# Optimization experiments

Hardware: AMD Instinct MI355X
Metric: run time of the kernel (lower is better)

The kernel has to match this reference:

```python
import jax, jax.numpy as jnp
import numpy as np

N = 100000      # num_nodes
E = 1600000     # num edges (avg degree 16)
R = 400         # num_relations passed to GCNLayer (masks at R and 2R)
DIN, DH, DOUT = 128, 128, 128
EPS = 1e-5


def setup_inputs() -> dict:
    key = jax.random.key(0)
    ks = jax.random.split(key, 8)
    src = jax.random.randint(ks[0], (E,), 0, N)
    dst = jax.random.randint(ks[1], (E,), 0, N)
    rel = jax.random.randint(ks[2], (E,), 0, 2 * R + 1)  # covers orig/inverse/self-loop buckets
    edges = jnp.stack([src, rel, dst], axis=1)  # [E,3] = (head, rel, tail)

    def xinit(k, shape, fan_in):
        return jax.random.normal(k, shape, jnp.float32) * (1.0 / np.sqrt(fan_in))

    node_emb = xinit(ks[3], (N, DIN), DIN)
    # stacked relation-branch linears: [3, out, in] = (original, inverse, self_loop)
    W1 = xinit(ks[4], (3, DH, DIN), DIN)
    b1 = jnp.zeros((3, DH), jnp.float32)
    Ws1 = xinit(ks[5], (DH, DIN), DIN)
    bs1 = jnp.zeros((DH,), jnp.float32)
    g1 = jnp.ones((DH,), jnp.float32)
    be1 = jnp.zeros((DH,), jnp.float32)
    W2 = xinit(ks[6], (3, DOUT, DH), DH)
    b2 = jnp.zeros((3, DOUT), jnp.float32)
    Ws2 = xinit(ks[7], (DOUT, DH), DH)
    bs2 = jnp.zeros((DOUT,), jnp.float32)
    g2 = jnp.ones((DOUT,), jnp.float32)
    be2 = jnp.zeros((DOUT,), jnp.float32)
    return dict(edges=edges, node_emb=node_emb, W1=W1, b1=b1, Ws1=Ws1, bs1=bs1,
                g1=g1, be1=be1, W2=W2, b2=b2, Ws2=Ws2, bs2=bs2, g2=g2, be2=be2)


def _gcn_layer(x, src, dst, bucket, W, b):
    # Project node features once per relation branch (same math as projecting
    # gathered src features, but N << E so this is cheaper): Y[r] = x @ W[r].T + b[r]
    Y = jnp.einsum('nd,rod->rno', x, W) + b[:, None, :]     # [3, N, out]
    msgs = Y[bucket, src]                                   # [E, out] gather by (branch, src)
    n = x.shape[0]
    out = jax.ops.segment_sum(msgs, dst, num_segments=n)    # scatter-add to dst
    cnt = jax.ops.segment_sum(jnp.ones_like(dst, dtype=x.dtype), dst, num_segments=n)
    out = out / jnp.maximum(cnt, 1.0)[:, None]              # degree norm, clamp min=1
    return jax.nn.relu(out)


def _layer_norm(x, g, b):
    m = jnp.mean(x, axis=-1, keepdims=True)
    v = jnp.mean((x - m) ** 2, axis=-1, keepdims=True)
    return (x - m) * jax.lax.rsqrt(v + EPS) * g + b


def reference(edges, node_emb, W1, b1, Ws1, bs1, g1, be1, W2, b2, Ws2, bs2, g2, be2):
    src, rel, dst = edges[:, 0], edges[:, 1], edges[:, 2]
    # bucket: 0=original (rel<R), 1=inverse (R<=rel<2R), 2=self-loop (rel>=2R)
    bucket = (rel >= R).astype(jnp.int32) + (rel >= 2 * R).astype(jnp.int32)

    x1 = _gcn_layer(node_emb, src, dst, bucket, W1, b1)
    x1 = x1 + node_emb @ Ws1.T + bs1                # skip1
    x1 = _layer_norm(x1, g1, be1)                   # dropout: eval-mode identity

    x2 = _gcn_layer(x1, src, dst, bucket, W2, b2)
    x2 = x2 + x1 @ Ws2.T + bs2                      # skip2
    x2 = _layer_norm(x2, g2, be2)
    return x2
```

## Files before the change

### kernel.cpp

```cpp
#include <hip/hip_runtime.h>
#include <stdint.h>

typedef unsigned int uint;
typedef unsigned short ushort;

#define NNODES 100000
#define NPAD   100096
#define NEDGES 1600000
#define RCONST 400
#define CAP    64
#define ZROW   NNODES

#define NBKT   196
#define NBLK_A 512
#define EPB    3125
#define RUNCAP 64

typedef __attribute__((ext_vector_type(8))) short short8;
typedef __attribute__((ext_vector_type(4))) float f32x4;

__device__ __forceinline__ float bflo(uint u){ union{uint i;float f;}c; c.i=u<<16; return c.f; }
__device__ __forceinline__ float bfhi(uint u){ union{uint i;float f;}c; c.i=u&0xFFFF0000u; return c.f; }
__device__ __forceinline__ ushort f2bf(float f){ union{uint i;float ff;}c; c.ff=f; uint u=c.i;
    return (ushort)((u + 0x7FFFu + ((u>>16)&1u))>>16); }
__device__ __forceinline__ uint pack2(float lo, float hi){
    return (uint)f2bf(lo) | ((uint)f2bf(hi)<<16); }


__global__ __launch_bounds__(256) void binfill_kernel(const int* __restrict__ edges,
                                                      int* __restrict__ runcnt,
                                                      uint* __restrict__ binned) {
    __shared__ int pos[NBKT];
    int blk = blockIdx.x, tid = threadIdx.x;
    for (int i = tid; i < NBKT; i += 256) pos[i] = 0;
    __syncthreads();
    int start = blk * EPB;
    for (int i = tid; i < EPB; i += 256) {
        int e = start + i;
        int src = edges[e * 3];
        int rel = edges[e * 3 + 1];
        int dst = edges[e * 3 + 2];
        int bkt = (rel >= RCONST) + (rel >= 2 * RCONST);
        int b = dst >> 9, off = dst & 511;
        int p = atomicAdd(&pos[b], 1);
        if (p < RUNCAP)
            binned[((size_t)b * NBLK_A + blk) * RUNCAP + p] =
                (uint)src | ((uint)bkt << 17) | ((uint)off << 19);
    }
    __syncthreads();
    for (int i = tid; i < NBKT; i += 256)
        runcnt[blk * NBKT + i] = min(pos[i], RUNCAP);
}


__global__ __launch_bounds__(256) void scatter_kernel(const uint* __restrict__ binned,
                                                      const int* __restrict__ runcnt,
                                                      int* __restrict__ elist,
                                                      uint* __restrict__ segp,
                                                      float4* __restrict__ cnts) {
    __shared__ int cnt3[512][4];
    __shared__ int cur[512][4];
    int b = blockIdx.x, tid = threadIdx.x;
    int base = b << 9;
    for (int i = tid; i < 512; i += 256) { cnt3[i][0] = 0; cnt3[i][1] = 0; cnt3[i][2] = 0; }
    __syncthreads();
    #pragma unroll
    for (int rr = 0; rr < 2; ++rr) {
        int r = tid * 2 + rr;
        int n = runcnt[r * NBKT + b];
        const uint* p = binned + ((size_t)b * NBLK_A + r) * RUNCAP;
        for (int i = 0; i < n; ++i) {
            uint e = p[i];
            atomicAdd(&cnt3[e >> 19][(e >> 17) & 3], 1);
        }
    }
    __syncthreads();
    for (int i = tid; i < 512; i += 256) {
        int node = base + i;
        if (node >= NPAD) continue;
        int c0 = cnt3[i][0], c1 = cnt3[i][1], c2 = cnt3[i][2];
        int n0 = min((c0 + 1) & ~1, 64);
        int n1 = min((c1 + 1) & ~1, 64 - n0);
        int n2 = min((c2 + 1) & ~1, 64 - n0 - n1);
        int s1 = n0, s2 = n0 + n1;
        cur[i][0] = 0; cur[i][1] = s1; cur[i][2] = s2;
        int* er = elist + (size_t)node * 64;
        for (int j = min(c0, n0); j < n0; ++j) er[j] = ZROW;
        for (int j = min(c1, n1); j < n1; ++j) er[s1 + j] = ZROW;
        for (int j = min(c2, n2); j < n2; ++j) er[s2 + j] = ZROW;
        cnt3[i][0] = s1; cnt3[i][1] = s2; cnt3[i][2] = s2 + n2;
        segp[node] = (uint)n0 | ((uint)n1 << 8) | ((uint)n2 << 16);
        float4 v;
        v.x = (float)c0; v.y = (float)c1; v.z = (float)c2;
        v.w = 1.0f / fmaxf((float)(c0 + c1 + c2), 1.0f);
        cnts[node] = v;
    }
    __syncthreads();
    #pragma unroll
    for (int rr = 0; rr < 2; ++rr) {
        int r = tid * 2 + rr;
        int n = runcnt[r * NBKT + b];
        const uint* p = binned + ((size_t)b * NBLK_A + r) * RUNCAP;
        for (int i = 0; i < n; ++i) {
            uint e = p[i];
            int off = (int)(e >> 19), bk = (int)((e >> 17) & 3);
            int pos = atomicAdd(&cur[off][bk], 1);
            if (pos < cnt3[off][bk])
                elist[(size_t)(base + off) * 64 + pos] = (int)(e & 0x7FFFFu);
        }
    }
}


__global__ __launch_bounds__(256) void convx_kernel(const float* __restrict__ x,
                                                    uint* __restrict__ xb) {
    size_t i = (size_t)blockIdx.x * 256 + threadIdx.x;
    if (i < (size_t)NPAD * 64) {
        uint val = 0;
        if (i < (size_t)NNODES * 64) {
            float2 f = *(const float2*)&x[i * 2];
            val = pack2(f.x, f.y);
        }
        xb[i] = val;
    }
}

__global__ __launch_bounds__(256) void wconv_kernel(const float* __restrict__ W,
                                                    const float* __restrict__ Ws,
                                                    uint* __restrict__ Wb) {
    int i = blockIdx.x * 256 + threadIdx.x;
    if (i < 128 * 256) {
        int n = i >> 8, kp = i & 255, k = kp * 2;
        float v0, v1;
        if (k < 384) {
            int r = k >> 7, kk = k & 127;
            const float* p = W + r * 16384 + n * 128 + kk;
            v0 = p[0]; v1 = p[1];
        } else {
            const float* p = Ws + n * 128 + (k - 384);
            v0 = p[0]; v1 = p[1];
        }
        Wb[i] = pack2(v0, v1);
    }
}


template<bool OUT_BF16>
__global__ __launch_bounds__(512, 2) void fused_kernel(
    const uint* __restrict__ xbu,
    const ushort* __restrict__ Wb,
    const uint* __restrict__ segp,
    const int*  __restrict__ elist,
    const float4* __restrict__ cnts,
    const float* __restrict__ bia,
    const float* __restrict__ bs,
    const float* __restrict__ g,
    const float* __restrict__ be,
    void* __restrict__ out) {
    __shared__ ushort lA[64 * 384];
    __shared__ ushort lB[128 * 64];
    __shared__ float sS1[4][64], sS2[4][64];
    __shared__ float sMean[64], sRstd[64];

    const ushort* xbs = (const ushort*)xbu;
    int tid = threadIdx.x;
    int w = tid >> 6, lane = tid & 63;
    int wm = w >> 2, wn = w & 3;
    int quad = lane >> 4, l15 = lane & 15;
    int node0 = blockIdx.x * 64;
    uint swzR = (uint)((l15 & 7) << 4);

    int brow = tid >> 2, bseg2 = (tid & 3) * 2;
    uint swzB = (uint)((brow & 7) << 4);
    uint4 rb0, rb1;
    auto loadB = [&](int t) {
        const ushort* pb = Wb + t * 64 + (size_t)brow * 512 + bseg2 * 8;
        rb0 = *(const uint4*)(pb);
        rb1 = *(const uint4*)(pb + 8);
    };
    auto storeB = [&]() {
        char* bB = (char*)lB + brow * 128;
        *(uint4*)(bB + (((uint)(bseg2 * 16)) ^ swzB))       = rb0;
        *(uint4*)(bB + (((uint)((bseg2 + 1) * 16)) ^ swzB)) = rb1;
    };

    loadB(0);

    for (int i = 0; i < 8; ++i) {
        int arow = w * 8 + i;
        int node = node0 + arow;
        uint sp = segp[node];
        int tot = (int)(sp & 255) + (int)((sp >> 8) & 255) + (int)((sp >> 16) & 255);
        float inv = cnts[node].w;
        int ve = elist[(size_t)node * 64 + lane];

        float a0l = 0.f, a0h = 0.f, a1l = 0.f, a1h = 0.f, a2l = 0.f, a2h = 0.f;
        int j = 0;
        for (; j + 4 <= tot; j += 4) {
            int e0 = __builtin_amdgcn_readlane(ve, j);
            int e1 = __builtin_amdgcn_readlane(ve, j + 1);
            int e2 = __builtin_amdgcn_readlane(ve, j + 2);
            int e3 = __builtin_amdgcn_readlane(ve, j + 3);
            int s0 = e0 & 0x1FFFF, k0 = e0 >> 17;
            int s1 = e1 & 0x1FFFF, k1 = e1 >> 17;
            int s2 = e2 & 0x1FFFF, k2 = e2 >> 17;
            int s3 = e3 & 0x1FFFF, k3 = e3 >> 17;
            uint u0 = xbu[((size_t)s0 << 6) + lane];
            uint u1 = xbu[((size_t)s1 << 6) + lane];
            uint u2 = xbu[((size_t)s2 << 6) + lane];
            uint u3 = xbu[((size_t)s3 << 6) + lane];

            float q00 = (k0 == 0) ? 1.f : 0.f, q01 = (k0 == 1) ? 1.f : 0.f, q02 = (k0 == 2) ? 1.f : 0.f;
            float q10 = (k1 == 0) ? 1.f : 0.f, q11 = (k1 == 1) ? 1.f : 0.f, q12 = (k1 == 2) ? 1.f : 0.f;
            float q20 = (k2 == 0) ? 1.f : 0.f, q21 = (k2 == 1) ? 1.f : 0.f, q22 = (k2 == 2) ? 1.f : 0.f;
            float q30 = (k3 == 0) ? 1.f : 0.f, q31 = (k3 == 1) ? 1.f : 0.f, q32 = (k3 == 2) ? 1.f : 0.f;

            float f0l = bflo(u0), f0h = bfhi(u0);
            float f1l = bflo(u1), f1h = bfhi(u1);
            float f2l = bflo(u2), f2h = bfhi(u2);
            float f3l = bflo(u3), f3h = bfhi(u3);

            a0l = fmaf(q00, f0l, a0l); a1l = fmaf(q01, f0l, a1l); a2l = fmaf(q02, f0l, a2l);
            a0h = fmaf(q00, f0h, a0h); a1h = fmaf(q01, f0h, a1h); a2h = fmaf(q02, f0h, a2h);
            a0l = fmaf(q10, f1l, a0l); a1l = fmaf(q11, f1l, a1l); a2l = fmaf(q12, f1l, a2l);
            a0h = fmaf(q10, f1h, a0h); a1h = fmaf(q11, f1h, a1h); a2h = fmaf(q12, f1h, a2h);
            a0l = fmaf(q20, f2l, a0l); a1l = fmaf(q21, f2l, a1l); a2l = fmaf(q22, f2l, a2l);
            a0h = fmaf(q20, f2h, a0h); a1h = fmaf(q21, f2h, a1h); a2h = fmaf(q22, f2h, a2h);
            a0l = fmaf(q30, f3l, a0l); a1l = fmaf(q31, f3l, a1l); a2l = fmaf(q32, f3l, a2l);
            a0h = fmaf(q30, f3h, a0h); a1h = fmaf(q31, f3h, a1h); a2h = fmaf(q32, f3h, a2h);
        }
        if (j < tot) {
            int e0 = __builtin_amdgcn_readlane(ve, j);
            int e1 = __builtin_amdgcn_readlane(ve, j + 1);
            int s0 = e0 & 0x1FFFF, k0 = e0 >> 17;
            int s1 = e1 & 0x1FFFF, k1 = e1 >> 17;
            uint u0 = xbu[((size_t)s0 << 6) + lane];
            uint u1 = xbu[((size_t)s1 << 6) + lane];
            float q00 = (k0 == 0) ? 1.f : 0.f, q01 = (k0 == 1) ? 1.f : 0.f, q02 = (k0 == 2) ? 1.f : 0.f;
            float q10 = (k1 == 0) ? 1.f : 0.f, q11 = (k1 == 1) ? 1.f : 0.f, q12 = (k1 == 2) ? 1.f : 0.f;
            float f0l = bflo(u0), f0h = bfhi(u0);
            float f1l = bflo(u1), f1h = bfhi(u1);
            a0l = fmaf(q00, f0l, a0l); a1l = fmaf(q01, f0l, a1l); a2l = fmaf(q02, f0l, a2l);
            a0h = fmaf(q00, f0h, a0h); a1h = fmaf(q01, f0h, a1h); a2h = fmaf(q02, f0h, a2h);
            a0l = fmaf(q10, f1l, a0l); a1l = fmaf(q11, f1l, a1l); a2l = fmaf(q12, f1l, a2l);
            a0h = fmaf(q10, f1h, a0h); a1h = fmaf(q11, f1h, a1h); a2h = fmaf(q12, f1h, a2h);
        }
        uint sw = (uint)((arow & 7) << 4);
        char* rA = (char*)lA + arow * 768;
        *(uint*)(rA + (((uint)(lane * 4)) ^ sw))       = pack2(a0l * inv, a0h * inv);
        *(uint*)(rA + (((uint)(256 + lane * 4)) ^ sw)) = pack2(a1l * inv, a1h * inv);
        *(uint*)(rA + (((uint)(512 + lane * 4)) ^ sw)) = pack2(a2l * inv, a2h * inv);
    }

    f32x4 accm[2][2], accq[2][2];
    f32x4 zero = {0.f, 0.f, 0.f, 0.f};
    #pragma unroll
    for (int i = 0; i < 2; ++i)
        #pragma unroll
        for (int j = 0; j < 2; ++j) { accm[i][j] = zero; accq[i][j] = zero; }

    __syncthreads();
    storeB();
    __syncthreads();

    #pragma unroll
    for (int kc = 0; kc < 8; ++kc) {
        if (kc < 7) loadB(kc + 1);
        #pragma unroll
        for (int ks = 0; ks < 2; ++ks) {
            short8 aF[2], bF[2];
            #pragma unroll
            for (int mt = 0; mt < 2; ++mt) {
                int row = wm * 32 + mt * 16 + l15;
                if (kc < 6)
                    aF[mt] = *(const short8*)((const char*)lA + row * 768 +
                        (((uint)((kc >> 1) * 256 + (kc & 1) * 128 + ks * 64 + quad * 16)) ^ swzR));
                else
                    aF[mt] = *(const short8*)(xbs + (size_t)(node0 + row) * 128 +
                                              (kc - 6) * 64 + ks * 32 + quad * 8);
            }
            #pragma unroll
            for (int nt = 0; nt < 2; ++nt) {
                int row = wn * 32 + nt * 16 + l15;
                bF[nt] = *(const short8*)((const char*)lB + row * 128 +
                                          (((uint)(ks * 64 + quad * 16)) ^ swzR));
            }
            #pragma unroll
            for (int mt = 0; mt < 2; ++mt)
                #pragma unroll
                for (int nt = 0; nt < 2; ++nt) {
                    if (kc < 6)
                        accm[mt][nt] = __builtin_amdgcn_mfma_f32_16x16x32_bf16(
                            aF[mt], bF[nt], accm[mt][nt], 0, 0, 0);
                    else
                        accq[mt][nt] = __builtin_amdgcn_mfma_f32_16x16x32_bf16(
                            aF[mt], bF[nt], accq[mt][nt], 0, 0, 0);
                }
        }
        if (kc < 7) { __syncthreads(); storeB(); __syncthreads(); }
    }

    int nl0 = wn * 32 + l15;
    float pb0[2], pb1[2], pb2[2], pbs[2], pg[2], pbe[2];
    #pragma unroll
    for (int nt = 0; nt < 2; ++nt) {
        int nl = nl0 + nt * 16;
        pb0[nt] = bia[nl]; pb1[nt] = bia[128 + nl]; pb2[nt] = bia[256 + nl];
        pbs[nt] = bs[nl];  pg[nt] = g[nl];          pbe[nt] = be[nl];
    }
    #pragma unroll
    for (int mt = 0; mt < 2; ++mt) {
        #pragma unroll
        for (int r = 0; r < 4; ++r) {
            int ml = wm * 32 + mt * 16 + quad * 4 + r;
            float4 c4 = cnts[node0 + ml];
            float s1 = 0.f, s2 = 0.f;
            #pragma unroll
            for (int nt = 0; nt < 2; ++nt) {
                float bd = (c4.x * pb0[nt] + c4.y * pb1[nt] + c4.z * pb2[nt]) * c4.w;
                float v = fmaxf(accm[mt][nt][r] + bd, 0.f) + accq[mt][nt][r] + pbs[nt];
                accm[mt][nt][r] = v;
                s1 += v; s2 += v * v;
            }
            #pragma unroll
            for (int mask = 1; mask < 16; mask <<= 1) {
                s1 += __shfl_xor(s1, mask);
                s2 += __shfl_xor(s2, mask);
            }
            if (l15 == 0) { sS1[wn][ml] = s1; sS2[wn][ml] = s2; }
        }
    }
    __syncthreads();
    if (tid < 64) {
        float s1 = sS1[0][tid] + sS1[1][tid] + sS1[2][tid] + sS1[3][tid];
        float s2 = sS2[0][tid] + sS2[1][tid] + sS2[2][tid] + sS2[3][tid];
        float mean = s1 * (1.f / 128.f);
        float var = s2 * (1.f / 128.f) - mean * mean;
        sMean[tid] = mean;
        sRstd[tid] = rsqrtf(var + 1e-5f);
    }
    __syncthreads();
    #pragma unroll
    for (int mt = 0; mt < 2; ++mt) {
        #pragma unroll
        for (int r = 0; r < 4; ++r) {
            int ml = wm * 32 + mt * 16 + quad * 4 + r;
            int node = node0 + ml;
            float mn = sMean[ml], rs = sRstd[ml];
            #pragma unroll
            for (int nt = 0; nt < 2; ++nt) {
                float v = (accm[mt][nt][r] - mn) * rs * pg[nt] + pbe[nt];
                if (OUT_BF16) {
                    float vh = __shfl_xor(v, 1);
                    if (!(l15 & 1)) {
                        uint val = (node < NNODES) ? pack2(v, vh) : 0u;
                        uint* o = (uint*)out;
                        o[(size_t)node * 64 + wn * 16 + nt * 8 + (l15 >> 1)] = val;
                    }
                } else {
                    if (node < NNODES) {
                        float* o = (float*)out;
                        o[(size_t)node * 128 + nl0 + nt * 16] = v;
                    }
                }
            }
        }
    }
}


extern "C" void kernel_launch(void* const* d_in, const int* in_sizes, int n_in,
                              void* d_out, int out_size, void* d_ws, size_t ws_size,
                              hipStream_t stream) {
    (void)in_sizes; (void)n_in; (void)out_size; (void)ws_size;

    const int*   edges = (const int*)d_in[0];
    const float* xemb  = (const float*)d_in[1];
    const float* W1  = (const float*)d_in[2];
    const float* b1  = (const float*)d_in[3];
    const float* Ws1 = (const float*)d_in[4];
    const float* bs1 = (const float*)d_in[5];
    const float* g1  = (const float*)d_in[6];
    const float* be1 = (const float*)d_in[7];
    const float* W2  = (const float*)d_in[8];
    const float* b2  = (const float*)d_in[9];
    const float* Ws2 = (const float*)d_in[10];
    const float* bs2 = (const float*)d_in[11];
    const float* g2  = (const float*)d_in[12];
    const float* be2 = (const float*)d_in[13];

    char* ws = (char*)d_ws;
    auto take = [&](size_t bytes) {
        char* p = ws;
        ws += (bytes + 255) & ~(size_t)255;
        return p;
    };
    int*    elist  = (int*)take((size_t)NPAD * CAP * 4);
    uint*   segp   = (uint*)take((size_t)NPAD * 4);
    float4* cnts   = (float4*)take((size_t)NPAD * 16);
    uint*   xb0    = (uint*)take((size_t)NPAD * 128 * 2);
    uint*   xb1    = (uint*)take((size_t)NPAD * 128 * 2);
    uint*   Wb1    = (uint*)take((size_t)128 * 512 * 2);
    uint*   Wb2    = (uint*)take((size_t)128 * 512 * 2);
    int*    runcnt = (int*)take((size_t)NBLK_A * NBKT * 4);
    uint*   binned = (uint*)take((size_t)NBKT * NBLK_A * RUNCAP * 4);

    binfill_kernel<<<NBLK_A, 256, 0, stream>>>(edges, runcnt, binned);
    scatter_kernel<<<NBKT, 256, 0, stream>>>(binned, runcnt, elist, segp, cnts);

    convx_kernel<<<(NPAD * 64) / 256, 256, 0, stream>>>(xemb, xb0);
    wconv_kernel<<<128, 256, 0, stream>>>(W1, Ws1, Wb1);
    wconv_kernel<<<128, 256, 0, stream>>>(W2, Ws2, Wb2);

    fused_kernel<true><<<NPAD / 64, 512, 0, stream>>>(
        xb0, (const ushort*)Wb1, segp, elist, cnts,
        b1, bs1, g1, be1, xb1);

    fused_kernel<false><<<NPAD / 64, 512, 0, stream>>>(
        xb1, (const ushort*)Wb2, segp, elist, cnts,
        b2, bs2, g2, be2, d_out);
}
```

Before: 448.1 us.

## Split fused gather+GEMM into separate gather and 128-row GEMM kernels, merge prep kernels

The fused per-layer kernel, which gathered neighbor aggregates into LDS and then ran the MFMA GEMM, is split in two. A gather kernel handles one node per wave, writes bf16 aggregates to a global buffer, and runs at full occupancy. A GEMM kernel with 128-row tiles then streams those aggregates and the skip features through LDS together with the weights. The scatter, x-conversion and weight-conversion kernels are merged into one launch to cut launch overhead. This adds a global round trip of roughly 77MB per layer in exchange for better latency hiding in the gather and less GEMM stalling.

After: 394.6 us. 11.9% less time.

```diff
diff --git a/kernel.cpp b/kernel.cpp
--- a/kernel.cpp
+++ b/kernel.cpp
@@ -15,6 +15,7 @@
 #define NBLK_A 512
 #define EPB    3125
 #define RUNCAP 64
+#define NCONVX 25024
 
 typedef __attribute__((ext_vector_type(8))) short short8;
 typedef __attribute__((ext_vector_type(4))) float f32x4;
@@ -53,83 +54,82 @@
 }
 
 
-__global__ __launch_bounds__(256) void scatter_kernel(const uint* __restrict__ binned,
-                                                      const int* __restrict__ runcnt,
-                                                      int* __restrict__ elist,
-                                                      uint* __restrict__ segp,
-                                                      float4* __restrict__ cnts) {
+__global__ __launch_bounds__(256) void scatterx_kernel(
+    const uint* __restrict__ binned, const int* __restrict__ runcnt,
+    int* __restrict__ elist, uint* __restrict__ segp, float4* __restrict__ cnts,
+    const float* __restrict__ x, uint* __restrict__ xb,
+    const float* __restrict__ W1, const float* __restrict__ Ws1, uint* __restrict__ Wb1,
+    const float* __restrict__ W2, const float* __restrict__ Ws2, uint* __restrict__ Wb2) {
     __shared__ int cnt3[512][4];
     __shared__ int cur[512][4];
-    int b = blockIdx.x, tid = threadIdx.x;
-    int base = b << 9;
-    for (int i = tid; i < 512; i += 256) { cnt3[i][0] = 0; cnt3[i][1] = 0; cnt3[i][2] = 0; }
-    __syncthreads();
-    #pragma unroll
-    for (int rr = 0; rr < 2; ++rr) {
-        int r = tid * 2 + rr;
-        int n = runcnt[r * NBKT + b];
-        const uint* p = binned + ((size_t)b * NBLK_A + r) * RUNCAP;
-        for (int i = 0; i < n; ++i) {
-            uint e = p[i];
-            atomicAdd(&cnt3[e >> 19][(e >> 17) & 3], 1);
-        }
-    }
-    __syncthreads();
-    for (int i = tid; i < 512; i += 256) {
-        int node = base + i;
-        if (node >= NPAD) continue;
-        int c0 = cnt3[i][0], c1 = cnt3[i][1], c2 = cnt3[i][2];
-        int n0 = min((c0 + 1) & ~1, 64);
-        int n1 = min((c1 + 1) & ~1, 64 - n0);
-        int n2 = min((c2 + 1) & ~1, 64 - n0 - n1);
-        int s1 = n0, s2 = n0 + n1;
-        cur[i][0] = 0; cur[i][1] = s1; cur[i][2] = s2;
-        int* er = elist + (size_t)node * 64;
-        for (int j = min(c0, n0); j < n0; ++j) er[j] = ZROW;
-        for (int j = min(c1, n1); j < n1; ++j) er[s1 + j] = ZROW;
-        for (int j = min(c2, n2); j < n2; ++j) er[s2 + j] = ZROW;
-        cnt3[i][0] = s1; cnt3[i][1] = s2; cnt3[i][2] = s2 + n2;
-        segp[node] = (uint)n0 | ((uint)n1 << 8) | ((uint)n2 << 16);
-        float4 v;
-        v.x = (float)c0; v.y = (float)c1; v.z = (float)c2;
-        v.w = 1.0f / fmaxf((float)(c0 + c1 + c2), 1.0f);
-        cnts[node] = v;
-    }
-    __syncthreads();
-    #pragma unroll
-    for (int rr = 0; rr < 2; ++rr) {
-        int r = tid * 2 + rr;
-        int n = runcnt[r * NBKT + b];
-        const uint* p = binned + ((size_t)b * NBLK_A + r) * RUNCAP;
-        for (int i = 0; i < n; ++i) {
-            uint e = p[i];
-            int off = (int)(e >> 19), bk = (int)((e >> 17) & 3);
-            int pos = atomicAdd(&cur[off][bk], 1);
-            if (pos < cnt3[off][bk])
-                elist[(size_t)(base + off) * 64 + pos] = (int)(e & 0x7FFFFu);
-        }
-    }
-}
-
-
-__global__ __launch_bounds__(256) void convx_kernel(const float* __restrict__ x,
-                                                    uint* __restrict__ xb) {
-    size_t i = (size_t)blockIdx.x * 256 + threadIdx.x;
-    if (i < (size_t)NPAD * 64) {
-        uint val = 0;
-        if (i < (size_t)NNODES * 64) {
-            float2 f = *(const float2*)&x[i * 2];
-            val = pack2(f.x, f.y);
-        }
-        xb[i] = val;
-    }
-}
-
-__global__ __launch_bounds__(256) void wconv_kernel(const float* __restrict__ W,
-                                                    const float* __restrict__ Ws,
-                                                    uint* __restrict__ Wb) {
-    int i = blockIdx.x * 256 + threadIdx.x;
-    if (i < 128 * 256) {
+    int blk = blockIdx.x, tid = threadIdx.x;
+
+    if (blk < NBKT) {
+        int b = blk;
+        int base = b << 9;
+        for (int i = tid; i < 512; i += 256) { cnt3[i][0] = 0; cnt3[i][1] = 0; cnt3[i][2] = 0; }
+        __syncthreads();
+        #pragma unroll
+        for (int rr = 0; rr < 2; ++rr) {
+            int r = tid * 2 + rr;
+            int n = runcnt[r * NBKT + b];
+            const uint* p = binned + ((size_t)b * NBLK_A + r) * RUNCAP;
+            for (int i = 0; i < n; ++i) {
+                uint e = p[i];
+                atomicAdd(&cnt3[e >> 19][(e >> 17) & 3], 1);
+            }
+        }
+        __syncthreads();
+        for (int i = tid; i < 512; i += 256) {
+            int node = base + i;
+            if (node >= NPAD) continue;
+            int c0 = cnt3[i][0], c1 = cnt3[i][1], c2 = cnt3[i][2];
+            int n0 = min((c0 + 1) & ~1, 64);
+            int n1 = min((c1 + 1) & ~1, 64 - n0);
+            int n2 = min((c2 + 1) & ~1, 64 - n0 - n1);
+            int s1 = n0, s2 = n0 + n1;
+            cur[i][0] = 0; cur[i][1] = s1; cur[i][2] = s2;
+            int* er = elist + (size_t)node * 64;
+            for (int j = min(c0, n0); j < n0; ++j) er[j] = ZROW;
+            for (int j = min(c1, n1); j < n1; ++j) er[s1 + j] = ZROW;
+            for (int j = min(c2, n2); j < n2; ++j) er[s2 + j] = ZROW;
+            cnt3[i][0] = s1; cnt3[i][1] = s2; cnt3[i][2] = s2 + n2;
+            segp[node] = (uint)n0 | ((uint)n1 << 8) | ((uint)n2 << 16);
+            float4 v;
+            v.x = (float)c0; v.y = (float)c1; v.z = (float)c2;
+            v.w = 1.0f / fmaxf((float)(c0 + c1 + c2), 1.0f);
+            cnts[node] = v;
+        }
+        __syncthreads();
+        #pragma unroll
+        for (int rr = 0; rr < 2; ++rr) {
+            int r = tid * 2 + rr;
+            int n = runcnt[r * NBKT + b];
+            const uint* p = binned + ((size_t)b * NBLK_A + r) * RUNCAP;
+            for (int i = 0; i < n; ++i) {
+                uint e = p[i];
+                int off = (int)(e >> 19), bk = (int)((e >> 17) & 3);
+                int pos = atomicAdd(&cur[off][bk], 1);
+                if (pos < cnt3[off][bk])
+                    elist[(size_t)(base + off) * 64 + pos] = (int)(e & 0x7FFFFu);
+            }
+        }
+    } else if (blk < NBKT + NCONVX) {
+        size_t i = (size_t)(blk - NBKT) * 256 + tid;
+        if (i < (size_t)NPAD * 64) {
+            uint val = 0;
+            if (i < (size_t)NNODES * 64) {
+                float2 f = *(const float2*)&x[i * 2];
+                val = pack2(f.x, f.y);
+            }
+            xb[i] = val;
+        }
+    } else {
+        int wi = blk - (NBKT + NCONVX);
+        const float* W  = (wi < 128) ? W1  : W2;
+        const float* Ws = (wi < 128) ? Ws1 : Ws2;
+        uint* Wb        = (wi < 128) ? Wb1 : Wb2;
+        int i = (wi & 127) * 256 + tid;
         int n = i >> 8, kp = i & 255, k = kp * 2;
         float v0, v1;
         if (k < 384) {
@@ -145,139 +145,135 @@
 }
 
 
-template<bool OUT_BF16>
-__global__ __launch_bounds__(512, 2) void fused_kernel(
+__global__ __launch_bounds__(256) void gather_kernel(
     const uint* __restrict__ xbu,
-    const ushort* __restrict__ Wb,
     const uint* __restrict__ segp,
     const int*  __restrict__ elist,
     const float4* __restrict__ cnts,
+    uint* __restrict__ Ab) {
+    int w = threadIdx.x >> 6, lane = threadIdx.x & 63;
+    int node = blockIdx.x * 4 + w;
+    uint sp = __builtin_amdgcn_readfirstlane(segp[node]);
+    int tot = (int)(sp & 255) + (int)((sp >> 8) & 255) + (int)((sp >> 16) & 255);
+    float inv = cnts[node].w;
+    int ve = elist[(size_t)node * 64 + lane];
+
+    float a0l = 0.f, a0h = 0.f, a1l = 0.f, a1h = 0.f, a2l = 0.f, a2h = 0.f;
+    int j = 0;
+    for (; j + 4 <= tot; j += 4) {
+        int e0 = __builtin_amdgcn_readlane(ve, j);
+        int e1 = __builtin_amdgcn_readlane(ve, j + 1);
+        int e2 = __builtin_amdgcn_readlane(ve, j + 2);
+        int e3 = __builtin_amdgcn_readlane(ve, j + 3);
+        int s0 = e0 & 0x1FFFF, k0 = e0 >> 17;
+        int s1 = e1 & 0x1FFFF, k1 = e1 >> 17;
+        int s2 = e2 & 0x1FFFF, k2 = e2 >> 17;
+        int s3 = e3 & 0x1FFFF, k3 = e3 >> 17;
+        uint u0 = xbu[((size_t)s0 << 6) + lane];
+        uint u1 = xbu[((size_t)s1 << 6) + lane];
+        uint u2 = xbu[((size_t)s2 << 6) + lane];
+        uint u3 = xbu[((size_t)s3 << 6) + lane];
+
+        float q00 = (k0 == 0) ? 1.f : 0.f, q01 = (k0 == 1) ? 1.f : 0.f, q02 = (k0 == 2) ? 1.f : 0.f;
+        float q10 = (k1 == 0) ? 1.f : 0.f, q11 = (k1 == 1) ? 1.f : 0.f, q12 = (k1 == 2) ? 1.f : 0.f;
+        float q20 = (k2 == 0) ? 1.f : 0.f, q21 = (k2 == 1) ? 1.f : 0.f, q22 = (k2 == 2) ? 1.f : 0.f;
+        float q30 = (k3 == 0) ? 1.f : 0.f, q31 = (k3 == 1) ? 1.f : 0.f, q32 = (k3 == 2) ? 1.f : 0.f;
+
+        float f0l = bflo(u0), f0h = bfhi(u0);
+        float f1l = bflo(u1), f1h = bfhi(u1);
+        float f2l = bflo(u2), f2h = bfhi(u2);
+        float f3l = bflo(u3), f3h = bfhi(u3);
+
+        a0l = fmaf(q00, f0l, a0l); a1l = fmaf(q01, f0l, a1l); a2l = fmaf(q02, f0l, a2l);
+        a0h = fmaf(q00, f0h, a0h); a1h = fmaf(q01, f0h, a1h); a2h = fmaf(q02, f0h, a2h);
+        a0l = fmaf(q10, f1l, a0l); a1l = fmaf(q11, f1l, a1l); a2l = fmaf(q12, f1l, a2l);
+        a0h = fmaf(q10, f1h, a0h); a1h = fmaf(q11, f1h, a1h); a2h = fmaf(q12, f1h, a2h);
+        a0l = fmaf(q20, f2l, a0l); a1l = fmaf(q21, f2l, a1l); a2l = fmaf(q22, f2l, a2l);
+        a0h = fmaf(q20, f2h, a0h); a1h = fmaf(q21, f2h, a1h); a2h = fmaf(q22, f2h, a2h);
+        a0l = fmaf(q30, f3l, a0l); a1l = fmaf(q31, f3l, a1l); a2l = fmaf(q32, f3l, a2l);
+        a0h = fmaf(q30, f3h, a0h); a1h = fmaf(q31, f3h, a1h); a2h = fmaf(q32, f3h, a2h);
+    }
+    if (j < tot) {
+        int e0 = __builtin_amdgcn_readlane(ve, j);
+        int e1 = __builtin_amdgcn_readlane(ve, j + 1);
+        int s0 = e0 & 0x1FFFF, k0 = e0 >> 17;
+        int s1 = e1 & 0x1FFFF, k1 = e1 >> 17;
+        uint u0 = xbu[((size_t)s0 << 6) + lane];
+        uint u1 = xbu[((size_t)s1 << 6) + lane];
+        float q00 = (k0 == 0) ? 1.f : 0.f, q01 = (k0 == 1) ? 1.f : 0.f, q02 = (k0 == 2) ? 1.f : 0.f;
+        float q10 = (k1 == 0) ? 1.f : 0.f, q11 = (k1 == 1) ? 1.f : 0.f, q12 = (k1 == 2) ? 1.f : 0.f;
+        float f0l = bflo(u0), f0h = bfhi(u0);
+        float f1l = bflo(u1), f1h = bfhi(u1);
+        a0l = fmaf(q00, f0l, a0l); a1l = fmaf(q01, f0l, a1l); a2l = fmaf(q02, f0l, a2l);
+        a0h = fmaf(q00, f0h, a0h); a1h = fmaf(q01, f0h, a1h); a2h = fmaf(q02, f0h, a2h);
+        a0l = fmaf(q10, f1l, a0l); a1l = fmaf(q11, f1l, a1l); a2l = fmaf(q12, f1l, a2l);
+        a0h = fmaf(q10, f1h, a0h); a1h = fmaf(q11, f1h, a1h); a2h = fmaf(q12, f1h, a2h);
+    }
+
+    size_t ab = (size_t)node * 192 + lane;
+    Ab[ab]       = pack2(a0l * inv, a0h * inv);
+    Ab[ab + 64]  = pack2(a1l * inv, a1h * inv);
+    Ab[ab + 128] = pack2(a2l * inv, a2h * inv);
+}
+
+
+template<bool OUT_BF16>
+__global__ __launch_bounds__(512, 2) void gemm_kernel(
+    const ushort* __restrict__ Ab,
+    const ushort* __restrict__ xb,
+    const ushort* __restrict__ Wb,
     const float* __restrict__ bia,
     const float* __restrict__ bs,
     const float* __restrict__ g,
     const float* __restrict__ be,
+    const float4* __restrict__ cnts,
     void* __restrict__ out) {
-    __shared__ ushort lA[64 * 384];
+    __shared__ ushort lA[128 * 64];
     __shared__ ushort lB[128 * 64];
-    __shared__ float sS1[4][64], sS2[4][64];
-    __shared__ float sMean[64], sRstd[64];
-
-    const ushort* xbs = (const ushort*)xbu;
+    __shared__ float sS1[4][128], sS2[4][128];
+    __shared__ float sMean[128], sRstd[128];
+
     int tid = threadIdx.x;
     int w = tid >> 6, lane = tid & 63;
     int wm = w >> 2, wn = w & 3;
     int quad = lane >> 4, l15 = lane & 15;
-    int node0 = blockIdx.x * 64;
+    int node0 = blockIdx.x * 128;
+
+    int srow = tid >> 2, sseg = (tid & 3) * 2;
+    uint swzS = (uint)((srow & 7) << 4);
     uint swzR = (uint)((l15 & 7) << 4);
 
-    int brow = tid >> 2, bseg2 = (tid & 3) * 2;
-    uint swzB = (uint)((brow & 7) << 4);
-    uint4 rb0, rb1;
-    auto loadB = [&](int t) {
-        const ushort* pb = Wb + t * 64 + (size_t)brow * 512 + bseg2 * 8;
+    const ushort* gA = Ab + (size_t)node0 * 384;
+    const ushort* gX = xb + (size_t)node0 * 128;
+
+    f32x4 accm[4][2], accq[4][2];
+    f32x4 zero = {0.f, 0.f, 0.f, 0.f};
+    #pragma unroll
+    for (int i = 0; i < 4; ++i)
+        #pragma unroll
+        for (int j = 0; j < 2; ++j) { accm[i][j] = zero; accq[i][j] = zero; }
+
+    uint4 ra0, ra1, rb0, rb1;
+    auto load_chunk = [&](int t) {
+        const ushort* srcA; size_t strA;
+        if (t < 6) { srcA = gA + t * 64;       strA = 384; }
+        else       { srcA = gX + (t - 6) * 64; strA = 128; }
+        const ushort* pa = srcA + (size_t)srow * strA + sseg * 8;
+        ra0 = *(const uint4*)(pa);
+        ra1 = *(const uint4*)(pa + 8);
+        const ushort* pb = Wb + t * 64 + (size_t)srow * 512 + sseg * 8;
         rb0 = *(const uint4*)(pb);
         rb1 = *(const uint4*)(pb + 8);
     };
-    auto storeB = [&]() {
-        char* bB = (char*)lB + brow * 128;
-        *(uint4*)(bB + (((uint)(bseg2 * 16)) ^ swzB))       = rb0;
-        *(uint4*)(bB + (((uint)((bseg2 + 1) * 16)) ^ swzB)) = rb1;
-    };
-
-    loadB(0);
-
-    for (int i = 0; i < 8; ++i) {
-        int arow = w * 8 + i;
-        int node = node0 + arow;
-        uint sp = segp[node];
-        int tot = (int)(sp & 255) + (int)((sp >> 8) & 255) + (int)((sp >> 16) & 255);
-        float inv = cnts[node].w;
-        int ve = elist[(size_t)node * 64 + lane];
-
-        float a0l = 0.f, a0h = 0.f, a1l = 0.f, a1h = 0.f, a2l = 0.f, a2h = 0.f;
-        int j = 0;
-        for (; j + 4 <= tot; j += 4) {
-            int e0 = __builtin_amdgcn_readlane(ve, j);
-            int e1 = __builtin_amdgcn_readlane(ve, j + 1);
-            int e2 = __builtin_amdgcn_readlane(ve, j + 2);
-            int e3 = __builtin_amdgcn_readlane(ve, j + 3);
-            int s0 = e0 & 0x1FFFF, k0 = e0 >> 17;
-            int s1 = e1 & 0x1FFFF, k1 = e1 >> 17;
-            int s2 = e2 & 0x1FFFF, k2 = e2 >> 17;
-            int s3 = e3 & 0x1FFFF, k3 = e3 >> 17;
-            uint u0 = xbu[((size_t)s0 << 6) + lane];
-            uint u1 = xbu[((size_t)s1 << 6) + lane];
-            uint u2 = xbu[((size_t)s2 << 6) + lane];
-            uint u3 = xbu[((size_t)s3 << 6) + lane];
-
-            float q00 = (k0 == 0) ? 1.f : 0.f, q01 = (k0 == 1) ? 1.f : 0.f, q02 = (k0 == 2) ? 1.f : 0.f;
-            float q10 = (k1 == 0) ? 1.f : 0.f, q11 = (k1 == 1) ? 1.f : 0.f, q12 = (k1 == 2) ? 1.f : 0.f;
-            float q20 = (k2 == 0) ? 1.f : 0.f, q21 = (k2 == 1) ? 1.f : 0.f, q22 = (k2 == 2) ? 1.f : 0.f;
-            float q30 = (k3 == 0) ? 1.f : 0.f, q31 = (k3 == 1) ? 1.f : 0.f, q32 = (k3 == 2) ? 1.f : 0.f;
-
-            float f0l = bflo(u0), f0h = bfhi(u0);
-            float f1l = bflo(u1), f1h = bfhi(u1);
-            float f2l = bflo(u2), f2h = bfhi(u2);
-            float f3l = bflo(u3), f3h = bfhi(u3);
-
-            a0l = fmaf(q00, f0l, a0l); a1l = fmaf(q01, f0l, a1l); a2l = fmaf(q02, f0l, a2l);
-            a0h = fmaf(q00, f0h, a0h); a1h = fmaf(q01, f0h, a1h); a2h = fmaf(q02, f0h, a2h);
-            a0l = fmaf(q10, f1l, a0l); a1l = fmaf(q11, f1l, a1l); a2l = fmaf(q12, f1l, a2l);
-            a0h = fmaf(q10, f1h, a0h); a1h = fmaf(q11, f1h, a1h); a2h = fmaf(q12, f1h, a2h);
-            a0l = fmaf(q20, f2l, a0l); a1l = fmaf(q21, f2l, a1l); a2l = fmaf(q22, f2l, a2l);
-            a0h = fmaf(q20, f2h, a0h); a1h = fmaf(q21, f2h, a1h); a2h = fmaf(q22, f2h, a2h);
-            a0l = fmaf(q30, f3l, a0l); a1l = fmaf(q31, f3l, a1l); a2l = fmaf(q32, f3l, a2l);
-            a0h = fmaf(q30, f3h, a0h); a1h = fmaf(q31, f3h, a1h); a2h = fmaf(q32, f3h, a2h);
-        }
-        if (j < tot) {
-            int e0 = __builtin_amdgcn_readlane(ve, j);
-            int e1 = __builtin_amdgcn_readlane(ve, j + 1);
-            int s0 = e0 & 0x1FFFF, k0 = e0 >> 17;
-            int s1 = e1 & 0x1FFFF, k1 = e1 >> 17;
-            uint u0 = xbu[((size_t)s0 << 6) + lane];
-            uint u1 = xbu[((size_t)s1 << 6) + lane];
-            float q00 = (k0 == 0) ? 1.f : 0.f, q01 = (k0 == 1) ? 1.f : 0.f, q02 = (k0 == 2) ? 1.f : 0.f;
-            float q10 = (k1 == 0) ? 1.f : 0.f, q11 = (k1 == 1) ? 1.f : 0.f, q12 = (k1 == 2) ? 1.f : 0.f;
-            float f0l = bflo(u0), f0h = bfhi(u0);
-            float f1l = bflo(u1), f1h = bfhi(u1);
-            a0l = fmaf(q00, f0l, a0l); a1l = fmaf(q01, f0l, a1l); a2l = fmaf(q02, f0l, a2l);
-            a0h = fmaf(q00, f0h, a0h); a1h = fmaf(q01, f0h, a1h); a2h = fmaf(q02, f0h, a2h);
-            a0l = fmaf(q10, f1l, a0l); a1l = fmaf(q11, f1l, a1l); a2l = fmaf(q12, f1l, a2l);
-            a0h = fmaf(q10, f1h, a0h); a1h = fmaf(q11, f1h, a1h); a2h = fmaf(q12, f1h, a2h);
-        }
-        uint sw = (uint)((arow & 7) << 4);
-        char* rA = (char*)lA + arow * 768;
-        *(uint*)(rA + (((uint)(lane * 4)) ^ sw))       = pack2(a0l * inv, a0h * inv);
-        *(uint*)(rA + (((uint)(256 + lane * 4)) ^ sw)) = pack2(a1l * inv, a1h * inv);
-        *(uint*)(rA + (((uint)(512 + lane * 4)) ^ sw)) = pack2(a2l * inv, a2h * inv);
-    }
-
-    f32x4 accm[2][2], accq[2][2];
-    f32x4 zero = {0.f, 0.f, 0.f, 0.f};
-    #pragma unroll
-    for (int i = 0; i < 2; ++i)
-        #pragma unroll
-        for (int j = 0; j < 2; ++j) { accm[i][j] = zero; accq[i][j] = zero; }
-
-    __syncthreads();
-    storeB();
-    __syncthreads();
-
-    #pragma unroll
-    for (int kc = 0; kc < 8; ++kc) {
-        if (kc < 7) loadB(kc + 1);
+    auto compute = [&](f32x4 (&acc)[4][2]) {
         #pragma unroll
         for (int ks = 0; ks < 2; ++ks) {
-            short8 aF[2], bF[2];
-            #pragma unroll
-            for (int mt = 0; mt < 2; ++mt) {
-                int row = wm * 32 + mt * 16 + l15;
-                if (kc < 6)
-                    aF[mt] = *(const short8*)((const char*)lA + row * 768 +
-                        (((uint)((kc >> 1) * 256 + (kc & 1) * 128 + ks * 64 + quad * 16)) ^ swzR));
-                else
-                    aF[mt] = *(const short8*)(xbs + (size_t)(node0 + row) * 128 +
-                                              (kc - 6) * 64 + ks * 32 + quad * 8);
+            short8 aF[4], bF[2];
+            #pragma unroll
+            for (int mt = 0; mt < 4; ++mt) {
+                int row = wm * 64 + mt * 16 + l15;
+                aF[mt] = *(const short8*)((const char*)lA + row * 128 +
+                                          (((uint)(ks * 64 + quad * 16)) ^ swzR));
             }
             #pragma unroll
             for (int nt = 0; nt < 2; ++nt) {
@@ -286,18 +282,28 @@
                                           (((uint)(ks * 64 + quad * 16)) ^ swzR));
             }
             #pragma unroll
-            for (int mt = 0; mt < 2; ++mt)
+            for (int mt = 0; mt < 4; ++mt)
                 #pragma unroll
-                for (int nt = 0; nt < 2; ++nt) {
-                    if (kc < 6)
-                        accm[mt][nt] = __builtin_amdgcn_mfma_f32_16x16x32_bf16(
-                            aF[mt], bF[nt], accm[mt][nt], 0, 0, 0);
-                    else
-                        accq[mt][nt] = __builtin_amdgcn_mfma_f32_16x16x32_bf16(
-                            aF[mt], bF[nt], accq[mt][nt], 0, 0, 0);
-                }
-        }
-        if (kc < 7) { __syncthreads(); storeB(); __syncthreads(); }
+                for (int nt = 0; nt < 2; ++nt)
+                    acc[mt][nt] = __builtin_amdgcn_mfma_f32_16x16x32_bf16(
+                        aF[mt], bF[nt], acc[mt][nt], 0, 0, 0);
+        }
+    };
+
+    load_chunk(0);
+    for (int t = 0; t < 8; ++t) {
+        if (t) __syncthreads();
+        {
+            char* bA = (char*)lA + srow * 128;
+            *(uint4*)(bA + (((uint)(sseg * 16)) ^ swzS))       = ra0;
+            *(uint4*)(bA + (((uint)((sseg + 1) * 16)) ^ swzS)) = ra1;
+            char* bB = (char*)lB + srow * 128;
+            *(uint4*)(bB + (((uint)(sseg * 16)) ^ swzS))       = rb0;
+            *(uint4*)(bB + (((uint)((sseg + 1) * 16)) ^ swzS)) = rb1;
+        }
+        __syncthreads();
+        if (t < 7) load_chunk(t + 1);
+        if (t < 6) compute(accm); else compute(accq);
     }
 
     int nl0 = wn * 32 + l15;
@@ -309,10 +315,10 @@
         pbs[nt] = bs[nl];  pg[nt] = g[nl];          pbe[nt] = be[nl];
     }
     #pragma unroll
-    for (int mt = 0; mt < 2; ++mt) {
+    for (int mt = 0; mt < 4; ++mt) {
         #pragma unroll
         for (int r = 0; r < 4; ++r) {
-            int ml = wm * 32 + mt * 16 + quad * 4 + r;
+            int ml = wm * 64 + mt * 16 + quad * 4 + r;
             float4 c4 = cnts[node0 + ml];
             float s1 = 0.f, s2 = 0.f;
             #pragma unroll
@@ -331,7 +337,7 @@
         }
     }
     __syncthreads();
-    if (tid < 64) {
+    if (tid < 128) {
         float s1 = sS1[0][tid] + sS1[1][tid] + sS1[2][tid] + sS1[3][tid];
         float s2 = sS2[0][tid] + sS2[1][tid] + sS2[2][tid] + sS2[3][tid];
         float mean = s1 * (1.f / 128.f);
@@ -341,10 +347,10 @@
     }
     __syncthreads();
     #pragma unroll
-    for (int mt = 0; mt < 2; ++mt) {
+    for (int mt = 0; mt < 4; ++mt) {
         #pragma unroll
         for (int r = 0; r < 4; ++r) {
-            int ml = wm * 32 + mt * 16 + quad * 4 + r;
+            int ml = wm * 64 + mt * 16 + quad * 4 + r;
             int node = node0 + ml;
             float mn = sMean[ml], rs = sRstd[ml];
             #pragma unroll
@@ -400,23 +406,24 @@
     float4* cnts   = (float4*)take((size_t)NPAD * 16);
     uint*   xb0    = (uint*)take((size_t)NPAD * 128 * 2);
     uint*   xb1    = (uint*)take((size_t)NPAD * 128 * 2);
+    uint*   Ab     = (uint*)take((size_t)NPAD * 384 * 2);
     uint*   Wb1    = (uint*)take((size_t)128 * 512 * 2);
     uint*   Wb2    = (uint*)take((size_t)128 * 512 * 2);
     int*    runcnt = (int*)take((size_t)NBLK_A * NBKT * 4);
     uint*   binned = (uint*)take((size_t)NBKT * NBLK_A * RUNCAP * 4);
 
     binfill_kernel<<<NBLK_A, 256, 0, stream>>>(edges, runcnt, binned);
-    scatter_kernel<<<NBKT, 256, 0, stream>>>(binned, runcnt, elist, segp, cnts);
-
-    convx_kernel<<<(NPAD * 64) / 256, 256, 0, stream>>>(xemb, xb0);
-    wconv_kernel<<<128, 256, 0, stream>>>(W1, Ws1, Wb1);
-    wconv_kernel<<<128, 256, 0, stream>>>(W2, Ws2, Wb2);
-
-    fused_kernel<true><<<NPAD / 64, 512, 0, stream>>>(
-        xb0, (const ushort*)Wb1, segp, elist, cnts,
-        b1, bs1, g1, be1, xb1);
-
-    fused_kernel<false><<<NPAD / 64, 512, 0, stream>>>(
-        xb1, (const ushort*)Wb2, segp, elist, cnts,
-        b2, bs2, g2, be2, d_out);
+    scatterx_kernel<<<NBKT + NCONVX + 256, 256, 0, stream>>>(
+        binned, runcnt, elist, segp, cnts,
+        xemb, xb0, W1, Ws1, Wb1, W2, Ws2, Wb2);
+
+    gather_kernel<<<NNODES / 4, 256, 0, stream>>>(xb0, segp, elist, cnts, Ab);
+    gemm_kernel<true><<<NPAD / 128, 512, 0, stream>>>(
+        (const ushort*)Ab, (const ushort*)xb0, (const ushort*)Wb1,
+        b1, bs1, g1, be1, cnts, xb1);
+
+    gather_kernel<<<NNODES / 4, 256, 0, stream>>>(xb1, segp, elist, cnts, Ab);
+    gemm_kernel<false><<<NPAD / 128, 512, 0, stream>>>(
+        (const ushort*)Ab, (const ushort*)xb1, (const ushort*)Wb2,
+        b2, bs2, g2, be2, cnts, d_out);
 }
```
